# Kernel optimization log

Measured on AMD Instinct MI355X. Metric: run time of the kernel, lower is better.

## Reference

```python
import jax, jax.numpy as jnp
import numpy as np
import math

B, T, C = 2, 2048, 768
N_HEAD, HEAD_DIM = 12, 64
TAU = 1.0
NEG_INF = -1e30  # stand-in for float('-inf') safe under softmax


def setup_inputs() -> dict:
    key = jax.random.key(0)
    k1, k2, k3, k4, k5 = jax.random.split(key, 5)
    hd = N_HEAD * HEAD_DIM
    x = jax.random.normal(k1, (B, T, C), dtype=jnp.float32)
    W_attn = jax.random.normal(k2, (C, 3 * hd), dtype=jnp.float32) * (1.0 / math.sqrt(C))
    b_attn = jnp.zeros((3 * hd,), dtype=jnp.float32)
    W_proj = jax.random.normal(k3, (hd, C), dtype=jnp.float32) * (1.0 / math.sqrt(hd))
    b_proj = jnp.zeros((C,), dtype=jnp.float32)
    return {"x": x, "W_attn": W_attn, "b_attn": b_attn, "W_proj": W_proj, "b_proj": b_proj}


def reference(x, W_attn, b_attn, W_proj, b_proj):
    Bs, Ts, Cs = x.shape
    hd = N_HEAD * HEAD_DIM
    qkv = x @ W_attn + b_attn                                  # [B,T,3*H*hd]
    q, k, v = jnp.split(qkv, 3, axis=2)
    q = q.reshape(Bs, Ts, N_HEAD, HEAD_DIM).transpose(0, 2, 1, 3)  # [B,H,T,d]
    k = k.reshape(Bs, Ts, N_HEAD, HEAD_DIM).transpose(0, 2, 1, 3)
    v = v.reshape(Bs, Ts, N_HEAD, HEAD_DIM).transpose(0, 2, 1, 3)

    att = jnp.einsum('bhtd,bhsd->bhts', q, k) * (1.0 / math.sqrt(HEAD_DIM))
    causal = jnp.tril(jnp.ones((Ts, Ts), dtype=bool))
    att = jnp.where(causal[None, None], att, NEG_INF)          # [B,H,T,T]

    # selection scores from head 0; relu(-inf) == 0 so masked entries vanish
    S = jax.nn.relu(att[:, 0])                                  # [B,T,T]
    # protect_bos_token: zero column 0
    S = S * (jnp.arange(Ts) > 0).astype(S.dtype)[None, None, :]
    # prevent_from_masking_myself: zero diagonal
    S = S * (1.0 - jnp.eye(Ts, dtype=S.dtype))[None]
    # roll rows down by 1 with zero row at the top
    S_shifted = jnp.concatenate([jnp.zeros_like(S[:, :1]), S[:, :-1]], axis=1)
    FF = jnp.cumsum(S_shifted, axis=1)[:, None]                 # [B,1,T,T]
    FF_sum = jnp.clip(FF, 0.0, TAU).sum(axis=-1)                # [B,1,T]
    positions = jnp.arange(Ts, dtype=jnp.float32).reshape(1, 1, Ts, 1)
    M = positions - FF_sum / TAU                                # broadcast -> [1,B,T,T]

    att = jax.nn.softmax(att - FF, axis=-1)
    y = jnp.einsum('bhts,bhsd->bhtd', att, v)
    y = y.transpose(0, 2, 1, 3).reshape(Bs, Ts, hd)
    y = y @ W_proj + b_proj
    return y, M
```

## Files before the change

kernel.cpp:

```cpp
#include <hip/hip_runtime.h>
#include <cstddef>

#define TB   2
#define TT   2048
#define TC   768
#define NHD  12
#define HDD  64
#define QKVN 2304
#define BTM  4096

#define FF_OFF   9437184ull
#define GSUM_OFF 17825792ull
#define FSUM_OFF 17891328ull
#define YATT_OFF 17895424ull
#define YSZ      3145728

typedef __attribute__((ext_vector_type(8))) short bf16x8;
typedef __attribute__((ext_vector_type(4))) float f32x4;

__device__ inline unsigned short f2bf(float f) {
    unsigned u = __float_as_uint(f);
    return (unsigned short)((u + 0x7fffu + ((u >> 16) & 1u)) >> 16);
}

__global__ __launch_bounds__(256) void castbf(
    const float* __restrict__ in, unsigned short* __restrict__ out, int n8)
{
    int idx = blockIdx.x * 256 + threadIdx.x;
    if (idx >= n8) return;
    const float4* p = (const float4*)(in + (size_t)idx * 8);
    float4 a = p[0], b = p[1];
    union { unsigned short us[8]; uint4 u4; } r;
    r.us[0] = f2bf(a.x); r.us[1] = f2bf(a.y); r.us[2] = f2bf(a.z); r.us[3] = f2bf(a.w);
    r.us[4] = f2bf(b.x); r.us[5] = f2bf(b.y); r.us[6] = f2bf(b.z); r.us[7] = f2bf(b.w);
    *(uint4*)(out + (size_t)idx * 8) = r.u4;
}

__global__ __launch_bounds__(256) void tcast(
    const float* __restrict__ W, unsigned short* __restrict__ Wt, int K, int N)
{
    __shared__ unsigned short T[64][80];
    const int tid = threadIdx.x;
    const int k0 = blockIdx.x * 64, n0 = blockIdx.y * 64;
#pragma unroll
    for (int u = 0; u < 4; ++u) {
        int f = u * 256 + tid;
        int kr = f >> 4, nc = (f & 15) * 4;
        float4 v = *(const float4*)(W + (size_t)(k0 + kr) * N + n0 + nc);
        T[nc + 0][kr] = f2bf(v.x); T[nc + 1][kr] = f2bf(v.y);
        T[nc + 2][kr] = f2bf(v.z); T[nc + 3][kr] = f2bf(v.w);
    }
    __syncthreads();
#pragma unroll
    for (int u = 0; u < 2; ++u) {
        int f = u * 256 + tid;
        int nr = f >> 3, kc = (f & 7) * 8;
        *(uint4*)(Wt + (size_t)(n0 + nr) * K + k0 + kc) = *(uint4*)&T[nr][kc];
    }
}

__global__ __launch_bounds__(256) void gemm_bf16(
    const unsigned short* __restrict__ A, const unsigned short* __restrict__ Bt,
    const float* __restrict__ bias, float* __restrict__ C,
    int M, int N, int K)
{
    __shared__ unsigned short As[128 * 64];
    __shared__ unsigned short Bs[128 * 64];
    const int tid = threadIdx.x;
    const int w = tid >> 6, lane = tid & 63;
    const int row0 = blockIdx.y * 128, col0 = blockIdx.x * 128;
    const int moff = (w >> 1) * 64, noff = (w & 1) * 64;
    const int lm = lane & 15, quad = lane >> 4;

    f32x4 acc[4][4];
#pragma unroll
    for (int i = 0; i < 4; ++i)
#pragma unroll
        for (int j = 0; j < 4; ++j) acc[i][j] = (f32x4){0.f, 0.f, 0.f, 0.f};

    for (int k0 = 0; k0 < K; k0 += 64) {
        __syncthreads();
#pragma unroll
        for (int u = 0; u < 4; ++u) {
            int unit = u * 256 + tid;
            int r = unit >> 3, kq = unit & 7;
            int kqs = kq ^ (r & 7);
            bf16x8 va = *(const bf16x8*)(A + (size_t)(row0 + r) * K + k0 + kq * 8);
            *(bf16x8*)&As[r * 64 + kqs * 8] = va;
            bf16x8 vb = *(const bf16x8*)(Bt + (size_t)(col0 + r) * K + k0 + kq * 8);
            *(bf16x8*)&Bs[r * 64 + kqs * 8] = vb;
        }
        __syncthreads();
#pragma unroll
        for (int kh = 0; kh < 2; ++kh) {
            const int kqb = kh * 4 + quad;
            bf16x8 af[4], bfr[4];
#pragma unroll
            for (int i = 0; i < 4; ++i) {
                int mr = moff + i * 16 + lm;
                af[i] = *(const bf16x8*)&As[mr * 64 + (kqb ^ (mr & 7)) * 8];
                int nr = noff + i * 16 + lm;
                bfr[i] = *(const bf16x8*)&Bs[nr * 64 + (kqb ^ (nr & 7)) * 8];
            }
#pragma unroll
            for (int i = 0; i < 4; ++i)
#pragma unroll
                for (int j = 0; j < 4; ++j)
                    acc[i][j] = __builtin_amdgcn_mfma_f32_16x16x32_bf16(
                        af[i], bfr[j], acc[i][j], 0, 0, 0);
        }
    }

#pragma unroll
    for (int j = 0; j < 4; ++j) {
        int n = col0 + noff + j * 16 + lm;
        float bv = bias[n];
#pragma unroll
        for (int i = 0; i < 4; ++i) {
            int mbase = row0 + moff + i * 16 + quad * 4;
#pragma unroll
            for (int r = 0; r < 4; ++r)
                C[(size_t)(mbase + r) * N + n] = acc[i][j][r] + bv;
        }
    }
}

__global__ __launch_bounds__(256) void s_head0_kernel(
    const float* __restrict__ qkv, float* __restrict__ S)
{
    const int tid = threadIdx.x;
    const int tx = tid & 15, ty = tid >> 4;
    const int s0 = blockIdx.x * 64, t0 = blockIdx.y * 64, b = blockIdx.z;

    if (s0 > t0 + 63) {
        float4 z = make_float4(0.f, 0.f, 0.f, 0.f);
#pragma unroll
        for (int i = 0; i < 4; ++i) {
            int t = t0 + ty * 4 + i;
            *(float4*)(S + ((size_t)b * TT + t) * TT + s0 + tx * 4) = z;
        }
        return;
    }

    __shared__ __align__(16) float As[16][68];
    __shared__ __align__(16) float Bs[16][68];
    float acc[4][4];
#pragma unroll
    for (int i = 0; i < 4; ++i)
#pragma unroll
        for (int j = 0; j < 4; ++j) acc[i][j] = 0.f;

    for (int k0 = 0; k0 < 64; k0 += 16) {
        int r = tid >> 2, c = (tid & 3) * 4;
        float4 av = *(const float4*)(qkv + ((size_t)b * TT + t0 + r) * QKVN + k0 + c);
        As[c + 0][r] = av.x; As[c + 1][r] = av.y;
        As[c + 2][r] = av.z; As[c + 3][r] = av.w;
        float4 bv = *(const float4*)(qkv + ((size_t)b * TT + s0 + r) * QKVN + 768 + k0 + c);
        Bs[c + 0][r] = bv.x; Bs[c + 1][r] = bv.y;
        Bs[c + 2][r] = bv.z; Bs[c + 3][r] = bv.w;
        __syncthreads();
#pragma unroll
        for (int kk = 0; kk < 16; ++kk) {
            float4 a4 = *(const float4*)&As[kk][ty * 4];
            float4 b4 = *(const float4*)&Bs[kk][tx * 4];
            float a[4] = {a4.x, a4.y, a4.z, a4.w};
            float bb[4] = {b4.x, b4.y, b4.z, b4.w};
#pragma unroll
            for (int i = 0; i < 4; ++i)
#pragma unroll
                for (int j = 0; j < 4; ++j)
                    acc[i][j] = fmaf(a[i], bb[j], acc[i][j]);
        }
        __syncthreads();
    }

#pragma unroll
    for (int i = 0; i < 4; ++i) {
        int t = t0 + ty * 4 + i;
        int sb = s0 + tx * 4;
        float4 o;
        o.x = (sb + 0 > 0 && sb + 0 < t) ? fmaxf(acc[i][0] * 0.125f, 0.f) : 0.f;
        o.y = (sb + 1 > 0 && sb + 1 < t) ? fmaxf(acc[i][1] * 0.125f, 0.f) : 0.f;
        o.z = (sb + 2 > 0 && sb + 2 < t) ? fmaxf(acc[i][2] * 0.125f, 0.f) : 0.f;
        o.w = (sb + 3 > 0 && sb + 3 < t) ? fmaxf(acc[i][3] * 0.125f, 0.f) : 0.f;
        *(float4*)(S + ((size_t)b * TT + t) * TT + sb) = o;
    }
}

__global__ void scan_pass1(const float* __restrict__ S, float* __restrict__ gsum)
{
    int s = blockIdx.x * 256 + threadIdx.x;
    int g = blockIdx.y, b = blockIdx.z;
    const float* base = S + ((size_t)b * TT + g * 128) * TT + s;
    float acc = 0.f;
#pragma unroll 4
    for (int r = 0; r < 128; ++r) acc += base[(size_t)r * TT];
    gsum[((size_t)b * 16 + g) * TT + s] = acc;
}

__global__ void scan_pass2(float* __restrict__ gsum)
{
    int idx = blockIdx.x * 256 + threadIdx.x;
    int b = idx >> 11, s = idx & 2047;
    float acc = 0.f;
#pragma unroll
    for (int g = 0; g < 16; ++g) {
        size_t a = ((size_t)b * 16 + g) * TT + s;
        float v = gsum[a];
        gsum[a] = acc;
        acc += v;
    }
}

__global__ void scan_pass3(float* __restrict__ S, const float* __restrict__ gsum)
{
    int s = blockIdx.x * 256 + threadIdx.x;
    int g = blockIdx.y, b = blockIdx.z;
    float acc = gsum[((size_t)b * 16 + g) * TT + s];
    float* base = S + ((size_t)b * TT + g * 128) * TT + s;
#pragma unroll 4
    for (int r = 0; r < 128; ++r) {
        float v = base[(size_t)r * TT];
        base[(size_t)r * TT] = acc;
        acc += v;
    }
}

__global__ void ffsum_kernel(const float* __restrict__ FF, float* __restrict__ FS)
{
    int row = blockIdx.x;
    int tid = threadIdx.x;
    const float* p = FF + (size_t)row * TT;
    float acc = 0.f;
#pragma unroll
    for (int s = tid; s < TT; s += 256) {
        float v = p[s];
        acc += fminf(fmaxf(v, 0.f), 1.f);
    }
#pragma unroll
    for (int off = 32; off > 0; off >>= 1) acc += __shfl_down(acc, off, 64);
    __shared__ float red[4];
    if ((tid & 63) == 0) red[tid >> 6] = acc;
    __syncthreads();
    if (tid == 0) FS[row] = (red[0] + red[1]) + (red[2] + red[3]);
}

__global__ void mout_kernel(const float* __restrict__ FS, float* __restrict__ Mo)
{
    size_t idx = (size_t)blockIdx.x * 256 + threadIdx.x;
    int j = (int)(idx & 2047);
    int i = (int)((idx >> 11) & 2047);
    int b = (int)(idx >> 22);
    Mo[idx] = (float)i - FS[b * TT + j];
}

__global__ __launch_bounds__(256) void attn_kernel(
    const float* __restrict__ qkv, const float* __restrict__ FF,
    unsigned short* __restrict__ Yb)
{
    const int sblk = blockIdx.x;
    const int hi = sblk >> 5;
    const int tt = (sblk ^ hi) & 31;
    const int h = hi % NHD;
    const int b = hi / NHD;

    const int tid = threadIdx.x;
    const int w = tid >> 6, lane = tid & 63;
    const int lm = lane & 15, quad = lane >> 4;
    const int t0 = tt * 64;

    __shared__ unsigned short Ks[64 * 64];
    __shared__ unsigned short Vt[64 * 64];
    __shared__ unsigned short Ps[64 * 64];

    const int tq = t0 + w * 16 + lm;
    bf16x8 qf[2];
#pragma unroll
    for (int kh = 0; kh < 2; ++kh) {
        const float* qp = qkv + ((size_t)(b * TT) + tq) * QKVN + h * 64 + kh * 32 + quad * 8;
        float4 a = *(const float4*)qp;
        float4 c = *(const float4*)(qp + 4);
        union { unsigned short us[8]; bf16x8 v; } u;
        u.us[0] = f2bf(a.x); u.us[1] = f2bf(a.y); u.us[2] = f2bf(a.z); u.us[3] = f2bf(a.w);
        u.us[4] = f2bf(c.x); u.us[5] = f2bf(c.y); u.us[6] = f2bf(c.z); u.us[7] = f2bf(c.w);
        qf[kh] = u.v;
    }

    f32x4 accO[4];
#pragma unroll
    for (int j = 0; j < 4; ++j) accO[j] = (f32x4){0.f, 0.f, 0.f, 0.f};
    float m_c = -3.0e38f, l_c = 0.f;

#pragma unroll 1
    for (int it = 0; it <= tt; ++it) {
        const int s0 = it * 64;
        __syncthreads();

#pragma unroll
        for (int u = 0; u < 2; ++u) {
            int unit = u * 256 + tid;
            int r = unit >> 3, kq = unit & 7;
            const float* kp = qkv + ((size_t)(b * TT) + s0 + r) * QKVN + 768 + h * 64 + kq * 8;
            float4 a = *(const float4*)kp;
            float4 c = *(const float4*)(kp + 4);
            union { unsigned short us[8]; bf16x8 v; } uu;
            uu.us[0] = f2bf(a.x); uu.us[1] = f2bf(a.y); uu.us[2] = f2bf(a.z); uu.us[3] = f2bf(a.w);
            uu.us[4] = f2bf(c.x); uu.us[5] = f2bf(c.y); uu.us[6] = f2bf(c.z); uu.us[7] = f2bf(c.w);
            *(bf16x8*)&Ks[r * 64 + (kq ^ (r & 7)) * 8] = uu.v;
        }
        {
            int s = lane;
            const float* vp = qkv + ((size_t)(b * TT) + s0 + s) * QKVN + 1536 + h * 64 + w * 16;
            float4 v0 = *(const float4*)(vp + 0);
            float4 v1 = *(const float4*)(vp + 4);
            float4 v2 = *(const float4*)(vp + 8);
            float4 v3 = *(const float4*)(vp + 12);
            float vv[16] = {v0.x, v0.y, v0.z, v0.w, v1.x, v1.y, v1.z, v1.w,
                            v2.x, v2.y, v2.z, v2.w, v3.x, v3.y, v3.z, v3.w};
            const int sg = s >> 3, sl = s & 7;
#pragma unroll
            for (int dd = 0; dd < 16; ++dd) {
                int d = w * 16 + dd;
                Vt[d * 64 + (sg ^ (d & 7)) * 8 + sl] = f2bf(vv[dd]);
            }
        }
        __syncthreads();

        f32x4 accS[4];
#pragma unroll
        for (int mi = 0; mi < 4; ++mi) accS[mi] = (f32x4){0.f, 0.f, 0.f, 0.f};
#pragma unroll
        for (int kh = 0; kh < 2; ++kh)
#pragma unroll
            for (int mi = 0; mi < 4; ++mi) {
                int sr = mi * 16 + lm;
                bf16x8 kf = *(const bf16x8*)&Ks[sr * 64 + ((kh * 4 + quad) ^ (sr & 7)) * 8];
                accS[mi] = __builtin_amdgcn_mfma_f32_16x16x32_bf16(kf, qf[kh], accS[mi], 0, 0, 0);
            }

        float sc[4][4];
        float rm = -3.0e38f;
        const float* ffrow = FF + ((size_t)(b * TT) + tq) * TT + s0;
#pragma unroll
        for (int mi = 0; mi < 4; ++mi) {
            float4 f4 = *(const float4*)(ffrow + mi * 16 + quad * 4);
            float fa[4] = {f4.x, f4.y, f4.z, f4.w};
#pragma unroll
            for (int r = 0; r < 4; ++r) {
                float v = accS[mi][r] * 0.125f - fa[r];
                if (it == tt && s0 + mi * 16 + quad * 4 + r > tq) v = -3.0e38f;
                sc[mi][r] = v;
                rm = fmaxf(rm, v);
            }
        }
        rm = fmaxf(rm, __shfl_xor(rm, 16, 64));
        rm = fmaxf(rm, __shfl_xor(rm, 32, 64));
        float mnew = fmaxf(m_c, rm);
        float alpha = __expf(m_c - mnew);
        m_c = mnew;
        float rs = 0.f;
#pragma unroll
        for (int mi = 0; mi < 4; ++mi)
#pragma unroll
            for (int r = 0; r < 4; ++r) {
                float p = __expf(sc[mi][r] - mnew);
                sc[mi][r] = p;
                rs += p;
            }
        rs += __shfl_xor(rs, 16, 64);
        rs += __shfl_xor(rs, 32, 64);
        l_c = l_c * alpha + rs;

        float a_r[4];
#pragma unroll
        for (int r = 0; r < 4; ++r) a_r[r] = __shfl(alpha, quad * 4 + r, 64);
#pragma unroll
        for (int nj = 0; nj < 4; ++nj)
#pragma unroll
            for (int r = 0; r < 4; ++r) accO[nj][r] *= a_r[r];

        const int qrow = w * 16 + lm;
#pragma unroll
        for (int mi = 0; mi < 4; ++mi)
#pragma unroll
            for (int r = 0; r < 4; ++r) {
                int sr = mi * 16 + quad * 4 + r;
                Ps[qrow * 64 + ((sr >> 3) ^ (qrow & 7)) * 8 + (sr & 7)] = f2bf(sc[mi][r]);
            }

        bf16x8 pf[2];
#pragma unroll
        for (int kh = 0; kh < 2; ++kh)
            pf[kh] = *(const bf16x8*)&Ps[qrow * 64 + ((kh * 4 + quad) ^ (qrow & 7)) * 8];
#pragma unroll
        for (int kh = 0; kh < 2; ++kh)
#pragma unroll
            for (int nj = 0; nj < 4; ++nj) {
                int dr = nj * 16 + lm;
                bf16x8 vf = *(const bf16x8*)&Vt[dr * 64 + ((kh * 4 + quad) ^ (dr & 7)) * 8];
                accO[nj] = __builtin_amdgcn_mfma_f32_16x16x32_bf16(pf[kh], vf, accO[nj], 0, 0, 0);
            }
    }

    float l_r[4];
#pragma unroll
    for (int r = 0; r < 4; ++r) l_r[r] = __shfl(l_c, quad * 4 + r, 64);
#pragma unroll
    for (int nj = 0; nj < 4; ++nj)
#pragma unroll
        for (int r = 0; r < 4; ++r) {
            int trow = t0 + w * 16 + quad * 4 + r;
            Yb[((size_t)(b * TT) + trow) * TC + h * 64 + nj * 16 + lm] =
                f2bf(accO[nj][r] / l_r[r]);
        }
}

extern "C" void kernel_launch(void* const* d_in, const int* in_sizes, int n_in,
                              void* d_out, int out_size, void* d_ws, size_t ws_size,
                              hipStream_t stream)
{
    const float* x      = (const float*)d_in[0];
    const float* W_attn = (const float*)d_in[1];
    const float* b_attn = (const float*)d_in[2];
    const float* W_proj = (const float*)d_in[3];
    const float* b_proj = (const float*)d_in[4];
    float* out = (float*)d_out;
    float* ws  = (float*)d_ws;

    float* qkv  = ws;
    float* FFb  = ws + FF_OFF;
    float* gsum = ws + GSUM_OFF;
    float* fsum = ws + FSUM_OFF;

    unsigned short* xb  = (unsigned short*)(ws + FF_OFF);
    unsigned short* WtA = xb + (size_t)BTM * TC;
    unsigned short* WtP = (unsigned short*)(ws + FF_OFF);
    unsigned short* ytb = (unsigned short*)(ws + YATT_OFF);

    castbf<<<dim3(1536), dim3(256), 0, stream>>>(x, xb, BTM * TC / 8);
    tcast<<<dim3(TC / 64, QKVN / 64), dim3(256), 0, stream>>>(W_attn, WtA, TC, QKVN);

    gemm_bf16<<<dim3(QKVN / 128, BTM / 128), dim3(256), 0, stream>>>(
        xb, WtA, b_attn, qkv, BTM, QKVN, TC);

    s_head0_kernel<<<dim3(TT / 64, TT / 64, TB), dim3(256), 0, stream>>>(qkv, FFb);

    scan_pass1<<<dim3(TT / 256, 16, TB), dim3(256), 0, stream>>>(FFb, gsum);
    scan_pass2<<<dim3(TB * TT / 256), dim3(256), 0, stream>>>(gsum);
    scan_pass3<<<dim3(TT / 256, 16, TB), dim3(256), 0, stream>>>(FFb, gsum);

    ffsum_kernel<<<dim3(TB * TT), dim3(256), 0, stream>>>(FFb, fsum);

    attn_kernel<<<dim3(TT / 64 * NHD * TB), dim3(256), 0, stream>>>(qkv, FFb, ytb);

    tcast<<<dim3(TC / 64, TC / 64), dim3(256), 0, stream>>>(W_proj, WtP, TC, TC);

    gemm_bf16<<<dim3(TC / 128, BTM / 128), dim3(256), 0, stream>>>(
        ytb, WtP, b_proj, out, BTM, TC, TC);

    mout_kernel<<<dim3((unsigned)((size_t)TB * TT * TT / 256)), dim3(256), 0, stream>>>(
        fsum, out + YSZ);
}
```

Baseline: 299.6 us.

## Fuse scan partial sums and clip-sum into S and scan kernels, widen attention tiles

The head-0 score kernel now uses bf16 MFMA and emits per-64-row column partial sums, which removes the separate scan_pass1 read of the full S matrix. The clip-and-sum row reduction is folded into scan_pass3 through wave shuffles and atomics, so the ffsum kernel and its extra pass over FF are gone. The attention kernel processes 128 query rows per block with two sub-tiles per wave, halving K/V staging per query and scheduling the heaviest blocks first. Risks are lower precision in S (bf16 instead of fp32 FMA), heavy atomic traffic on fsum, and fewer attention blocks (384) for occupancy.

```diff
diff --git a/kernel.cpp b/kernel.cpp
--- a/kernel.cpp
+++ b/kernel.cpp
@@ -10,9 +10,9 @@
 #define BTM  4096
 
 #define FF_OFF   9437184ull
-#define GSUM_OFF 17825792ull
-#define FSUM_OFF 17891328ull
-#define YATT_OFF 17895424ull
+#define YTB_OFF  17825792ull
+#define GSUM_OFF 19398656ull
+#define FSUM_OFF 19529728ull
 #define YSZ      3145728
 
 typedef __attribute__((ext_vector_type(8))) short bf16x8;
@@ -126,123 +126,124 @@
 }
 
 __global__ __launch_bounds__(256) void s_head0_kernel(
-    const float* __restrict__ qkv, float* __restrict__ S)
-{
+    const float* __restrict__ qkv, float* __restrict__ S, float* __restrict__ gsum)
+{
+    const int s0 = blockIdx.x * 64, t0 = blockIdx.y * 64, b = blockIdx.z;
     const int tid = threadIdx.x;
-    const int tx = tid & 15, ty = tid >> 4;
-    const int s0 = blockIdx.x * 64, t0 = blockIdx.y * 64, b = blockIdx.z;
-
-    if (s0 > t0 + 63) {
+    const int w = tid >> 6, lane = tid & 63;
+    const int lm = lane & 15, quad = lane >> 4;
+
+    if (s0 > t0) {
         float4 z = make_float4(0.f, 0.f, 0.f, 0.f);
 #pragma unroll
         for (int i = 0; i < 4; ++i) {
-            int t = t0 + ty * 4 + i;
-            *(float4*)(S + ((size_t)b * TT + t) * TT + s0 + tx * 4) = z;
-        }
+            int f = i * 256 + tid;
+            int r = f >> 4, c = (f & 15) * 4;
+            *(float4*)(S + ((size_t)b * TT + t0 + r) * TT + s0 + c) = z;
+        }
+        if (tid < 64) gsum[((size_t)b * 32 + blockIdx.y) * TT + s0 + tid] = 0.f;
         return;
     }
 
-    __shared__ __align__(16) float As[16][68];
-    __shared__ __align__(16) float Bs[16][68];
-    float acc[4][4];
-#pragma unroll
-    for (int i = 0; i < 4; ++i)
-#pragma unroll
-        for (int j = 0; j < 4; ++j) acc[i][j] = 0.f;
-
-    for (int k0 = 0; k0 < 64; k0 += 16) {
-        int r = tid >> 2, c = (tid & 3) * 4;
-        float4 av = *(const float4*)(qkv + ((size_t)b * TT + t0 + r) * QKVN + k0 + c);
-        As[c + 0][r] = av.x; As[c + 1][r] = av.y;
-        As[c + 2][r] = av.z; As[c + 3][r] = av.w;
-        float4 bv = *(const float4*)(qkv + ((size_t)b * TT + s0 + r) * QKVN + 768 + k0 + c);
-        Bs[c + 0][r] = bv.x; Bs[c + 1][r] = bv.y;
-        Bs[c + 2][r] = bv.z; Bs[c + 3][r] = bv.w;
-        __syncthreads();
-#pragma unroll
-        for (int kk = 0; kk < 16; ++kk) {
-            float4 a4 = *(const float4*)&As[kk][ty * 4];
-            float4 b4 = *(const float4*)&Bs[kk][tx * 4];
-            float a[4] = {a4.x, a4.y, a4.z, a4.w};
-            float bb[4] = {b4.x, b4.y, b4.z, b4.w};
-#pragma unroll
-            for (int i = 0; i < 4; ++i)
-#pragma unroll
-                for (int j = 0; j < 4; ++j)
-                    acc[i][j] = fmaf(a[i], bb[j], acc[i][j]);
-        }
-        __syncthreads();
-    }
-
-#pragma unroll
-    for (int i = 0; i < 4; ++i) {
-        int t = t0 + ty * 4 + i;
-        int sb = s0 + tx * 4;
-        float4 o;
-        o.x = (sb + 0 > 0 && sb + 0 < t) ? fmaxf(acc[i][0] * 0.125f, 0.f) : 0.f;
-        o.y = (sb + 1 > 0 && sb + 1 < t) ? fmaxf(acc[i][1] * 0.125f, 0.f) : 0.f;
-        o.z = (sb + 2 > 0 && sb + 2 < t) ? fmaxf(acc[i][2] * 0.125f, 0.f) : 0.f;
-        o.w = (sb + 3 > 0 && sb + 3 < t) ? fmaxf(acc[i][3] * 0.125f, 0.f) : 0.f;
-        *(float4*)(S + ((size_t)b * TT + t) * TT + sb) = o;
-    }
-}
-
-__global__ void scan_pass1(const float* __restrict__ S, float* __restrict__ gsum)
-{
-    int s = blockIdx.x * 256 + threadIdx.x;
-    int g = blockIdx.y, b = blockIdx.z;
-    const float* base = S + ((size_t)b * TT + g * 128) * TT + s;
-    float acc = 0.f;
-#pragma unroll 4
-    for (int r = 0; r < 128; ++r) acc += base[(size_t)r * TT];
-    gsum[((size_t)b * 16 + g) * TT + s] = acc;
-}
-
-__global__ void scan_pass2(float* __restrict__ gsum)
+    __shared__ unsigned short Ks[64 * 64];
+    __shared__ float colpart[4][64];
+
+#pragma unroll
+    for (int u = 0; u < 2; ++u) {
+        int unit = u * 256 + tid;
+        int r = unit >> 3, kq = unit & 7;
+        const float* kp = qkv + ((size_t)(b * TT) + s0 + r) * QKVN + 768 + kq * 8;
+        float4 a = *(const float4*)kp;
+        float4 c = *(const float4*)(kp + 4);
+        union { unsigned short us[8]; bf16x8 v; } uu;
+        uu.us[0] = f2bf(a.x); uu.us[1] = f2bf(a.y); uu.us[2] = f2bf(a.z); uu.us[3] = f2bf(a.w);
+        uu.us[4] = f2bf(c.x); uu.us[5] = f2bf(c.y); uu.us[6] = f2bf(c.z); uu.us[7] = f2bf(c.w);
+        *(bf16x8*)&Ks[r * 64 + (kq ^ (r & 7)) * 8] = uu.v;
+    }
+    bf16x8 af[2];
+#pragma unroll
+    for (int kh = 0; kh < 2; ++kh) {
+        const float* qp = qkv + ((size_t)(b * TT) + t0 + w * 16 + lm) * QKVN + kh * 32 + quad * 8;
+        float4 a = *(const float4*)qp;
+        float4 c = *(const float4*)(qp + 4);
+        union { unsigned short us[8]; bf16x8 v; } uu;
+        uu.us[0] = f2bf(a.x); uu.us[1] = f2bf(a.y); uu.us[2] = f2bf(a.z); uu.us[3] = f2bf(a.w);
+        uu.us[4] = f2bf(c.x); uu.us[5] = f2bf(c.y); uu.us[6] = f2bf(c.z); uu.us[7] = f2bf(c.w);
+        af[kh] = uu.v;
+    }
+    __syncthreads();
+
+    f32x4 acc[4];
+#pragma unroll
+    for (int nj = 0; nj < 4; ++nj) acc[nj] = (f32x4){0.f, 0.f, 0.f, 0.f};
+#pragma unroll
+    for (int kh = 0; kh < 2; ++kh)
+#pragma unroll
+        for (int nj = 0; nj < 4; ++nj) {
+            int sr = nj * 16 + lm;
+            bf16x8 kb = *(const bf16x8*)&Ks[sr * 64 + ((kh * 4 + quad) ^ (sr & 7)) * 8];
+            acc[nj] = __builtin_amdgcn_mfma_f32_16x16x32_bf16(af[kh], kb, acc[nj], 0, 0, 0);
+        }
+
+#pragma unroll
+    for (int nj = 0; nj < 4; ++nj) {
+        int s = s0 + nj * 16 + lm;
+        float cs = 0.f;
+#pragma unroll
+        for (int r = 0; r < 4; ++r) {
+            int t = t0 + w * 16 + quad * 4 + r;
+            float v = (s > 0 && s < t) ? fmaxf(acc[nj][r] * 0.125f, 0.f) : 0.f;
+            S[((size_t)b * TT + t) * TT + s] = v;
+            cs += v;
+        }
+        cs += __shfl_xor(cs, 16, 64);
+        cs += __shfl_xor(cs, 32, 64);
+        if (quad == 0) colpart[w][nj * 16 + lm] = cs;
+    }
+    __syncthreads();
+    if (tid < 64) {
+        float g = colpart[0][tid] + colpart[1][tid] + colpart[2][tid] + colpart[3][tid];
+        gsum[((size_t)b * 32 + blockIdx.y) * TT + s0 + tid] = g;
+    }
+}
+
+__global__ void scan_pass2(float* __restrict__ gsum, float* __restrict__ fsum)
 {
     int idx = blockIdx.x * 256 + threadIdx.x;
     int b = idx >> 11, s = idx & 2047;
+    fsum[idx] = 0.f;
     float acc = 0.f;
 #pragma unroll
-    for (int g = 0; g < 16; ++g) {
-        size_t a = ((size_t)b * 16 + g) * TT + s;
+    for (int g = 0; g < 32; ++g) {
+        size_t a = ((size_t)b * 32 + g) * TT + s;
         float v = gsum[a];
         gsum[a] = acc;
         acc += v;
     }
 }
 
-__global__ void scan_pass3(float* __restrict__ S, const float* __restrict__ gsum)
+__global__ void scan_pass3(float* __restrict__ S, const float* __restrict__ gsum,
+                           float* __restrict__ fsum)
 {
     int s = blockIdx.x * 256 + threadIdx.x;
     int g = blockIdx.y, b = blockIdx.z;
-    float acc = gsum[((size_t)b * 16 + g) * TT + s];
-    float* base = S + ((size_t)b * TT + g * 128) * TT + s;
-#pragma unroll 4
-    for (int r = 0; r < 128; ++r) {
+    int lane = threadIdx.x & 63;
+    float acc = gsum[((size_t)b * 32 + g) * TT + s];
+    float* base = S + ((size_t)b * TT + g * 64) * TT + s;
+#pragma unroll 2
+    for (int r = 0; r < 64; ++r) {
         float v = base[(size_t)r * TT];
         base[(size_t)r * TT] = acc;
+        float c = fminf(fmaxf(acc, 0.f), 1.f);
+        c += __shfl_xor(c, 1, 64);
+        c += __shfl_xor(c, 2, 64);
+        c += __shfl_xor(c, 4, 64);
+        c += __shfl_xor(c, 8, 64);
+        c += __shfl_xor(c, 16, 64);
+        c += __shfl_xor(c, 32, 64);
+        if (lane == 0) atomicAdd(&fsum[(size_t)b * TT + g * 64 + r], c);
         acc += v;
     }
-}
-
-__global__ void ffsum_kernel(const float* __restrict__ FF, float* __restrict__ FS)
-{
-    int row = blockIdx.x;
-    int tid = threadIdx.x;
-    const float* p = FF + (size_t)row * TT;
-    float acc = 0.f;
-#pragma unroll
-    for (int s = tid; s < TT; s += 256) {
-        float v = p[s];
-        acc += fminf(fmaxf(v, 0.f), 1.f);
-    }
-#pragma unroll
-    for (int off = 32; off > 0; off >>= 1) acc += __shfl_down(acc, off, 64);
-    __shared__ float red[4];
-    if ((tid & 63) == 0) red[tid >> 6] = acc;
-    __syncthreads();
-    if (tid == 0) FS[row] = (red[0] + red[1]) + (red[2] + red[3]);
 }
 
 __global__ void mout_kernel(const float* __restrict__ FS, float* __restrict__ Mo)
@@ -258,41 +259,47 @@
     const float* __restrict__ qkv, const float* __restrict__ FF,
     unsigned short* __restrict__ Yb)
 {
-    const int sblk = blockIdx.x;
-    const int hi = sblk >> 5;
-    const int tt = (sblk ^ hi) & 31;
-    const int h = hi % NHD;
-    const int b = hi / NHD;
+    const int x = blockIdx.x;
+    const int qb = 15 - x / 24;
+    const int bh = x % 24;
+    const int h = bh % NHD, b = bh / NHD;
+    const int t0 = qb * 128;
 
     const int tid = threadIdx.x;
     const int w = tid >> 6, lane = tid & 63;
     const int lm = lane & 15, quad = lane >> 4;
-    const int t0 = tt * 64;
 
     __shared__ unsigned short Ks[64 * 64];
     __shared__ unsigned short Vt[64 * 64];
-    __shared__ unsigned short Ps[64 * 64];
-
-    const int tq = t0 + w * 16 + lm;
-    bf16x8 qf[2];
-#pragma unroll
-    for (int kh = 0; kh < 2; ++kh) {
-        const float* qp = qkv + ((size_t)(b * TT) + tq) * QKVN + h * 64 + kh * 32 + quad * 8;
-        float4 a = *(const float4*)qp;
-        float4 c = *(const float4*)(qp + 4);
-        union { unsigned short us[8]; bf16x8 v; } u;
-        u.us[0] = f2bf(a.x); u.us[1] = f2bf(a.y); u.us[2] = f2bf(a.z); u.us[3] = f2bf(a.w);
-        u.us[4] = f2bf(c.x); u.us[5] = f2bf(c.y); u.us[6] = f2bf(c.z); u.us[7] = f2bf(c.w);
-        qf[kh] = u.v;
-    }
-
-    f32x4 accO[4];
-#pragma unroll
-    for (int j = 0; j < 4; ++j) accO[j] = (f32x4){0.f, 0.f, 0.f, 0.f};
-    float m_c = -3.0e38f, l_c = 0.f;
-
+    __shared__ unsigned short Ps[128 * 64];
+
+    bf16x8 qf[2][2];
+    int tq[2];
+#pragma unroll
+    for (int qs = 0; qs < 2; ++qs) {
+        tq[qs] = t0 + w * 32 + qs * 16 + lm;
+#pragma unroll
+        for (int kh = 0; kh < 2; ++kh) {
+            const float* qp = qkv + ((size_t)(b * TT) + tq[qs]) * QKVN + h * 64 + kh * 32 + quad * 8;
+            float4 a = *(const float4*)qp;
+            float4 c = *(const float4*)(qp + 4);
+            union { unsigned short us[8]; bf16x8 v; } u;
+            u.us[0] = f2bf(a.x); u.us[1] = f2bf(a.y); u.us[2] = f2bf(a.z); u.us[3] = f2bf(a.w);
+            u.us[4] = f2bf(c.x); u.us[5] = f2bf(c.y); u.us[6] = f2bf(c.z); u.us[7] = f2bf(c.w);
+            qf[qs][kh] = u.v;
+        }
+    }
+
+    f32x4 accO[2][4];
+#pragma unroll
+    for (int m = 0; m < 2; ++m)
+#pragma unroll
+        for (int j = 0; j < 4; ++j) accO[m][j] = (f32x4){0.f, 0.f, 0.f, 0.f};
+    float m_c[2] = {-3.0e38f, -3.0e38f}, l_c[2] = {0.f, 0.f};
+
+    const int ntile = qb * 2 + 2;
 #pragma unroll 1
-    for (int it = 0; it <= tt; ++it) {
+    for (int it = 0; it < ntile; ++it) {
         const int s0 = it * 64;
         __syncthreads();
 
@@ -326,93 +333,110 @@
         }
         __syncthreads();
 
-        f32x4 accS[4];
-#pragma unroll
-        for (int mi = 0; mi < 4; ++mi) accS[mi] = (f32x4){0.f, 0.f, 0.f, 0.f};
-#pragma unroll
-        for (int kh = 0; kh < 2; ++kh)
+        float alpha[2];
+#pragma unroll
+        for (int qs = 0; qs < 2; ++qs) {
+            f32x4 accS[4];
+#pragma unroll
+            for (int mi = 0; mi < 4; ++mi) accS[mi] = (f32x4){0.f, 0.f, 0.f, 0.f};
+#pragma unroll
+            for (int kh = 0; kh < 2; ++kh)
+#pragma unroll
+                for (int mi = 0; mi < 4; ++mi) {
+                    int sr = mi * 16 + lm;
+                    bf16x8 kf = *(const bf16x8*)&Ks[sr * 64 + ((kh * 4 + quad) ^ (sr & 7)) * 8];
+                    accS[mi] = __builtin_amdgcn_mfma_f32_16x16x32_bf16(kf, qf[qs][kh], accS[mi], 0, 0, 0);
+                }
+
+            float sc[4][4];
+            float rm = -3.0e38f;
+            const float* ffrow = FF + ((size_t)(b * TT) + tq[qs]) * TT + s0;
+            const bool diag = (it >= qb * 2);
 #pragma unroll
             for (int mi = 0; mi < 4; ++mi) {
-                int sr = mi * 16 + lm;
-                bf16x8 kf = *(const bf16x8*)&Ks[sr * 64 + ((kh * 4 + quad) ^ (sr & 7)) * 8];
-                accS[mi] = __builtin_amdgcn_mfma_f32_16x16x32_bf16(kf, qf[kh], accS[mi], 0, 0, 0);
-            }
-
-        float sc[4][4];
-        float rm = -3.0e38f;
-        const float* ffrow = FF + ((size_t)(b * TT) + tq) * TT + s0;
-#pragma unroll
-        for (int mi = 0; mi < 4; ++mi) {
-            float4 f4 = *(const float4*)(ffrow + mi * 16 + quad * 4);
-            float fa[4] = {f4.x, f4.y, f4.z, f4.w};
-#pragma unroll
-            for (int r = 0; r < 4; ++r) {
-                float v = accS[mi][r] * 0.125f - fa[r];
-                if (it == tt && s0 + mi * 16 + quad * 4 + r > tq) v = -3.0e38f;
-                sc[mi][r] = v;
-                rm = fmaxf(rm, v);
-            }
-        }
-        rm = fmaxf(rm, __shfl_xor(rm, 16, 64));
-        rm = fmaxf(rm, __shfl_xor(rm, 32, 64));
-        float mnew = fmaxf(m_c, rm);
-        float alpha = __expf(m_c - mnew);
-        m_c = mnew;
-        float rs = 0.f;
-#pragma unroll
-        for (int mi = 0; mi < 4; ++mi)
-#pragma unroll
-            for (int r = 0; r < 4; ++r) {
-                float p = __expf(sc[mi][r] - mnew);
-                sc[mi][r] = p;
-                rs += p;
-            }
-        rs += __shfl_xor(rs, 16, 64);
-        rs += __shfl_xor(rs, 32, 64);
-        l_c = l_c * alpha + rs;
-
-        float a_r[4];
-#pragma unroll
-        for (int r = 0; r < 4; ++r) a_r[r] = __shfl(alpha, quad * 4 + r, 64);
-#pragma unroll
-        for (int nj = 0; nj < 4; ++nj)
-#pragma unroll
-            for (int r = 0; r < 4; ++r) accO[nj][r] *= a_r[r];
-
-        const int qrow = w * 16 + lm;
-#pragma unroll
-        for (int mi = 0; mi < 4; ++mi)
-#pragma unroll
-            for (int r = 0; r < 4; ++r) {
-                int sr = mi * 16 + quad * 4 + r;
-                Ps[qrow * 64 + ((sr >> 3) ^ (qrow & 7)) * 8 + (sr & 7)] = f2bf(sc[mi][r]);
-            }
-
-        bf16x8 pf[2];
-#pragma unroll
-        for (int kh = 0; kh < 2; ++kh)
-            pf[kh] = *(const bf16x8*)&Ps[qrow * 64 + ((kh * 4 + quad) ^ (qrow & 7)) * 8];
+                float4 f4 = *(const float4*)(ffrow + mi * 16 + quad * 4);
+                float fa[4] = {f4.x, f4.y, f4.z, f4.w};
+#pragma unroll
+                for (int r = 0; r < 4; ++r) {
+                    float v = accS[mi][r] * 0.125f - fa[r];
+                    if (diag && s0 + mi * 16 + quad * 4 + r > tq[qs]) v = -3.0e38f;
+                    sc[mi][r] = v;
+                    rm = fmaxf(rm, v);
+                }
+            }
+            rm = fmaxf(rm, __shfl_xor(rm, 16, 64));
+            rm = fmaxf(rm, __shfl_xor(rm, 32, 64));
+            float mnew = fmaxf(m_c[qs], rm);
+            alpha[qs] = __expf(m_c[qs] - mnew);
+            m_c[qs] = mnew;
+            float rs = 0.f;
+#pragma unroll
+            for (int mi = 0; mi < 4; ++mi)
+#pragma unroll
+                for (int r = 0; r < 4; ++r) {
+                    float p = __expf(sc[mi][r] - mnew);
+                    sc[mi][r] = p;
+                    rs += p;
+                }
+            rs += __shfl_xor(rs, 16, 64);
+            rs += __shfl_xor(rs, 32, 64);
+            l_c[qs] = l_c[qs] * alpha[qs] + rs;
+
+            const int qrow = w * 32 + qs * 16 + lm;
+#pragma unroll
+            for (int mi = 0; mi < 4; ++mi)
+#pragma unroll
+                for (int r = 0; r < 4; ++r) {
+                    int sr = mi * 16 + quad * 4 + r;
+                    Ps[qrow * 64 + ((sr >> 3) ^ (qrow & 7)) * 8 + (sr & 7)] = f2bf(sc[mi][r]);
+                }
+        }
+
+#pragma unroll
+        for (int m = 0; m < 2; ++m) {
+            float a_r[4];
+#pragma unroll
+            for (int r = 0; r < 4; ++r) a_r[r] = __shfl(alpha[m], quad * 4 + r, 64);
+#pragma unroll
+            for (int nj = 0; nj < 4; ++nj)
+#pragma unroll
+                for (int r = 0; r < 4; ++r) accO[m][nj][r] *= a_r[r];
+        }
+
+        bf16x8 pf[2][2];
+#pragma unroll
+        for (int m = 0; m < 2; ++m)
+#pragma unroll
+            for (int kh = 0; kh < 2; ++kh) {
+                int qrow = w * 32 + m * 16 + lm;
+                pf[m][kh] = *(const bf16x8*)&Ps[qrow * 64 + ((kh * 4 + quad) ^ (qrow & 7)) * 8];
+            }
 #pragma unroll
         for (int kh = 0; kh < 2; ++kh)
 #pragma unroll
             for (int nj = 0; nj < 4; ++nj) {
                 int dr = nj * 16 + lm;
                 bf16x8 vf = *(const bf16x8*)&Vt[dr * 64 + ((kh * 4 + quad) ^ (dr & 7)) * 8];
-                accO[nj] = __builtin_amdgcn_mfma_f32_16x16x32_bf16(pf[kh], vf, accO[nj], 0, 0, 0);
-            }
-    }
-
-    float l_r[4];
-#pragma unroll
-    for (int r = 0; r < 4; ++r) l_r[r] = __shfl(l_c, quad * 4 + r, 64);
-#pragma unroll
-    for (int nj = 0; nj < 4; ++nj)
-#pragma unroll
-        for (int r = 0; r < 4; ++r) {
-            int trow = t0 + w * 16 + quad * 4 + r;
-            Yb[((size_t)(b * TT) + trow) * TC + h * 64 + nj * 16 + lm] =
-                f2bf(accO[nj][r] / l_r[r]);
-        }
+#pragma unroll
+                for (int m = 0; m < 2; ++m)
+                    accO[m][nj] = __builtin_amdgcn_mfma_f32_16x16x32_bf16(pf[m][kh], vf, accO[m][nj], 0, 0, 0);
+            }
+    }
+
+#pragma unroll
+    for (int m = 0; m < 2; ++m) {
+        float l_r[4];
+#pragma unroll
+        for (int r = 0; r < 4; ++r) l_r[r] = __shfl(l_c[m], quad * 4 + r, 64);
+#pragma unroll
+        for (int nj = 0; nj < 4; ++nj)
+#pragma unroll
+            for (int r = 0; r < 4; ++r) {
+                int trow = t0 + w * 32 + m * 16 + quad * 4 + r;
+                Yb[((size_t)(b * TT) + trow) * TC + h * 64 + nj * 16 + lm] =
+                    f2bf(accO[m][nj][r] / l_r[r]);
+            }
+    }
 }
 
 extern "C" void kernel_launch(void* const* d_in, const int* in_sizes, int n_in,
@@ -435,7 +459,7 @@
     unsigned short* xb  = (unsigned short*)(ws + FF_OFF);
     unsigned short* WtA = xb + (size_t)BTM * TC;
     unsigned short* WtP = (unsigned short*)(ws + FF_OFF);
-    unsigned short* ytb = (unsigned short*)(ws + YATT_OFF);
+    unsigned short* ytb = (unsigned short*)(ws + YTB_OFF);
 
     castbf<<<dim3(1536), dim3(256), 0, stream>>>(x, xb, BTM * TC / 8);
     tcast<<<dim3(TC / 64, QKVN / 64), dim3(256), 0, stream>>>(W_attn, WtA, TC, QKVN);
@@ -443,15 +467,12 @@
     gemm_bf16<<<dim3(QKVN / 128, BTM / 128), dim3(256), 0, stream>>>(
         xb, WtA, b_attn, qkv, BTM, QKVN, TC);
 
-    s_head0_kernel<<<dim3(TT / 64, TT / 64, TB), dim3(256), 0, stream>>>(qkv, FFb);
-
-    scan_pass1<<<dim3(TT / 256, 16, TB), dim3(256), 0, stream>>>(FFb, gsum);
-    scan_pass2<<<dim3(TB * TT / 256), dim3(256), 0, stream>>>(gsum);
-    scan_pass3<<<dim3(TT / 256, 16, TB), dim3(256), 0, stream>>>(FFb, gsum);
-
-    ffsum_kernel<<<dim3(TB * TT), dim3(256), 0, stream>>>(FFb, fsum);
-
-    attn_kernel<<<dim3(TT / 64 * NHD * TB), dim3(256), 0, stream>>>(qkv, FFb, ytb);
+    s_head0_kernel<<<dim3(TT / 64, TT / 64, TB), dim3(256), 0, stream>>>(qkv, FFb, gsum);
+
+    scan_pass2<<<dim3(TB * TT / 256), dim3(256), 0, stream>>>(gsum, fsum);
+    scan_pass3<<<dim3(TT / 256, 32, TB), dim3(256), 0, stream>>>(FFb, gsum, fsum);
+
+    attn_kernel<<<dim3(16 * NHD * TB), dim3(256), 0, stream>>>(qkv, FFb, ytb);
 
     tcast<<<dim3(TC / 64, TC / 64), dim3(256), 0, stream>>>(W_proj, WtP, TC, TC);
 
```

Measured after the change: 309.1 us. 3.2% more time.

## Store QKV as bf16, use MFMA for head-0 scores, fuse scan pass1

Applied to the files above, without the earlier changes.

The QKV GEMM now writes bf16 output directly, so attention and the selection-score kernels load bf16 without per-element conversion and QKV traffic is halved. The head-0 score kernel is rewritten to use bf16 MFMA instead of scalar FP32 FMAs, and it emits per-64-row column partial sums, which removes the separate scan_pass1 read over the full S matrix. The scan now uses 32 groups of 64 rows. The trade-off is that head-0 scores are computed from bf16-rounded q/k, which affects the precision of FF and M.

```diff
diff --git a/kernel.cpp b/kernel.cpp
--- a/kernel.cpp
+++ b/kernel.cpp
@@ -10,9 +10,9 @@
 #define BTM  4096
 
 #define FF_OFF   9437184ull
-#define GSUM_OFF 17825792ull
-#define FSUM_OFF 17891328ull
-#define YATT_OFF 17895424ull
+#define YTB_OFF  17825792ull
+#define GSUM_OFF 19398656ull
+#define FSUM_OFF 19529728ull
 #define YSZ      3145728
 
 typedef __attribute__((ext_vector_type(8))) short bf16x8;
@@ -59,10 +59,11 @@
     }
 }
 
+template <bool BF16OUT>
 __global__ __launch_bounds__(256) void gemm_bf16(
     const unsigned short* __restrict__ A, const unsigned short* __restrict__ Bt,
     const float* __restrict__ bias, float* __restrict__ C,
-    int M, int N, int K)
+    unsigned short* __restrict__ Cb, int M, int N, int K)
 {
     __shared__ unsigned short As[128 * 64];
     __shared__ unsigned short Bs[128 * 64];
@@ -119,83 +120,86 @@
         for (int i = 0; i < 4; ++i) {
             int mbase = row0 + moff + i * 16 + quad * 4;
 #pragma unroll
-            for (int r = 0; r < 4; ++r)
-                C[(size_t)(mbase + r) * N + n] = acc[i][j][r] + bv;
+            for (int r = 0; r < 4; ++r) {
+                float v = acc[i][j][r] + bv;
+                if (BF16OUT)
+                    Cb[(size_t)(mbase + r) * N + n] = f2bf(v);
+                else
+                    C[(size_t)(mbase + r) * N + n] = v;
+            }
         }
     }
 }
 
 __global__ __launch_bounds__(256) void s_head0_kernel(
-    const float* __restrict__ qkv, float* __restrict__ S)
-{
+    const unsigned short* __restrict__ qkvb, float* __restrict__ S,
+    float* __restrict__ gsum)
+{
+    const int s0 = blockIdx.x * 64, t0 = blockIdx.y * 64, b = blockIdx.z;
     const int tid = threadIdx.x;
-    const int tx = tid & 15, ty = tid >> 4;
-    const int s0 = blockIdx.x * 64, t0 = blockIdx.y * 64, b = blockIdx.z;
-
-    if (s0 > t0 + 63) {
+    const int w = tid >> 6, lane = tid & 63;
+    const int lm = lane & 15, quad = lane >> 4;
+
+    if (s0 > t0) {
         float4 z = make_float4(0.f, 0.f, 0.f, 0.f);
 #pragma unroll
         for (int i = 0; i < 4; ++i) {
-            int t = t0 + ty * 4 + i;
-            *(float4*)(S + ((size_t)b * TT + t) * TT + s0 + tx * 4) = z;
-        }
+            int f = i * 256 + tid;
+            int r = f >> 4, c = (f & 15) * 4;
+            *(float4*)(S + ((size_t)b * TT + t0 + r) * TT + s0 + c) = z;
+        }
+        if (tid < 64) gsum[((size_t)b * 32 + blockIdx.y) * TT + s0 + tid] = 0.f;
         return;
     }
 
-    __shared__ __align__(16) float As[16][68];
-    __shared__ __align__(16) float Bs[16][68];
-    float acc[4][4];
-#pragma unroll
-    for (int i = 0; i < 4; ++i)
-#pragma unroll
-        for (int j = 0; j < 4; ++j) acc[i][j] = 0.f;
-
-    for (int k0 = 0; k0 < 64; k0 += 16) {
-        int r = tid >> 2, c = (tid & 3) * 4;
-        float4 av = *(const float4*)(qkv + ((size_t)b * TT + t0 + r) * QKVN + k0 + c);
-        As[c + 0][r] = av.x; As[c + 1][r] = av.y;
-        As[c + 2][r] = av.z; As[c + 3][r] = av.w;
-        float4 bv = *(const float4*)(qkv + ((size_t)b * TT + s0 + r) * QKVN + 768 + k0 + c);
-        Bs[c + 0][r] = bv.x; Bs[c + 1][r] = bv.y;
-        Bs[c + 2][r] = bv.z; Bs[c + 3][r] = bv.w;
-        __syncthreads();
-#pragma unroll
-        for (int kk = 0; kk < 16; ++kk) {
-            float4 a4 = *(const float4*)&As[kk][ty * 4];
-            float4 b4 = *(const float4*)&Bs[kk][tx * 4];
-            float a[4] = {a4.x, a4.y, a4.z, a4.w};
-            float bb[4] = {b4.x, b4.y, b4.z, b4.w};
-#pragma unroll
-            for (int i = 0; i < 4; ++i)
-#pragma unroll
-                for (int j = 0; j < 4; ++j)
-                    acc[i][j] = fmaf(a[i], bb[j], acc[i][j]);
-        }
-        __syncthreads();
-    }
-
-#pragma unroll
-    for (int i = 0; i < 4; ++i) {
-        int t = t0 + ty * 4 + i;
-        int sb = s0 + tx * 4;
-        float4 o;
-        o.x = (sb + 0 > 0 && sb + 0 < t) ? fmaxf(acc[i][0] * 0.125f, 0.f) : 0.f;
-        o.y = (sb + 1 > 0 && sb + 1 < t) ? fmaxf(acc[i][1] * 0.125f, 0.f) : 0.f;
-        o.z = (sb + 2 > 0 && sb + 2 < t) ? fmaxf(acc[i][2] * 0.125f, 0.f) : 0.f;
-        o.w = (sb + 3 > 0 && sb + 3 < t) ? fmaxf(acc[i][3] * 0.125f, 0.f) : 0.f;
-        *(float4*)(S + ((size_t)b * TT + t) * TT + sb) = o;
-    }
-}
-
-__global__ void scan_pass1(const float* __restrict__ S, float* __restrict__ gsum)
-{
-    int s = blockIdx.x * 256 + threadIdx.x;
-    int g = blockIdx.y, b = blockIdx.z;
-    const float* base = S + ((size_t)b * TT + g * 128) * TT + s;
-    float acc = 0.f;
-#pragma unroll 4
-    for (int r = 0; r < 128; ++r) acc += base[(size_t)r * TT];
-    gsum[((size_t)b * 16 + g) * TT + s] = acc;
+    __shared__ unsigned short Ks[64 * 64];
+    __shared__ float colpart[4][64];
+
+#pragma unroll
+    for (int u = 0; u < 2; ++u) {
+        int unit = u * 256 + tid;
+        int r = unit >> 3, kq = unit & 7;
+        bf16x8 kv = *(const bf16x8*)(qkvb + ((size_t)(b * TT) + s0 + r) * QKVN + 768 + kq * 8);
+        *(bf16x8*)&Ks[r * 64 + (kq ^ (r & 7)) * 8] = kv;
+    }
+    bf16x8 af[2];
+#pragma unroll
+    for (int kh = 0; kh < 2; ++kh)
+        af[kh] = *(const bf16x8*)(qkvb + ((size_t)(b * TT) + t0 + w * 16 + lm) * QKVN + kh * 32 + quad * 8);
+    __syncthreads();
+
+    f32x4 acc[4];
+#pragma unroll
+    for (int nj = 0; nj < 4; ++nj) acc[nj] = (f32x4){0.f, 0.f, 0.f, 0.f};
+#pragma unroll
+    for (int kh = 0; kh < 2; ++kh)
+#pragma unroll
+        for (int nj = 0; nj < 4; ++nj) {
+            int sr = nj * 16 + lm;
+            bf16x8 kb = *(const bf16x8*)&Ks[sr * 64 + ((kh * 4 + quad) ^ (sr & 7)) * 8];
+            acc[nj] = __builtin_amdgcn_mfma_f32_16x16x32_bf16(af[kh], kb, acc[nj], 0, 0, 0);
+        }
+
+#pragma unroll
+    for (int nj = 0; nj < 4; ++nj) {
+        int s = s0 + nj * 16 + lm;
+        float cs = 0.f;
+#pragma unroll
+        for (int r = 0; r < 4; ++r) {
+            int t = t0 + w * 16 + quad * 4 + r;
+            float v = (s > 0 && s < t) ? fmaxf(acc[nj][r] * 0.125f, 0.f) : 0.f;
+            S[((size_t)b * TT + t) * TT + s] = v;
+            cs += v;
+        }
+        cs += __shfl_xor(cs, 16, 64);
+        cs += __shfl_xor(cs, 32, 64);
+        if (quad == 0) colpart[w][nj * 16 + lm] = cs;
+    }
+    __syncthreads();
+    if (tid < 64) {
+        float g = colpart[0][tid] + colpart[1][tid] + colpart[2][tid] + colpart[3][tid];
+        gsum[((size_t)b * 32 + blockIdx.y) * TT + s0 + tid] = g;
+    }
 }
 
 __global__ void scan_pass2(float* __restrict__ gsum)
@@ -204,8 +208,8 @@
     int b = idx >> 11, s = idx & 2047;
     float acc = 0.f;
 #pragma unroll
-    for (int g = 0; g < 16; ++g) {
-        size_t a = ((size_t)b * 16 + g) * TT + s;
+    for (int g = 0; g < 32; ++g) {
+        size_t a = ((size_t)b * 32 + g) * TT + s;
         float v = gsum[a];
         gsum[a] = acc;
         acc += v;
@@ -216,10 +220,10 @@
 {
     int s = blockIdx.x * 256 + threadIdx.x;
     int g = blockIdx.y, b = blockIdx.z;
-    float acc = gsum[((size_t)b * 16 + g) * TT + s];
-    float* base = S + ((size_t)b * TT + g * 128) * TT + s;
+    float acc = gsum[((size_t)b * 32 + g) * TT + s];
+    float* base = S + ((size_t)b * TT + g * 64) * TT + s;
 #pragma unroll 4
-    for (int r = 0; r < 128; ++r) {
+    for (int r = 0; r < 64; ++r) {
         float v = base[(size_t)r * TT];
         base[(size_t)r * TT] = acc;
         acc += v;
@@ -255,7 +259,7 @@
 }
 
 __global__ __launch_bounds__(256) void attn_kernel(
-    const float* __restrict__ qkv, const float* __restrict__ FF,
+    const unsigned short* __restrict__ qkvb, const float* __restrict__ FF,
     unsigned short* __restrict__ Yb)
 {
     const int sblk = blockIdx.x;
@@ -276,15 +280,8 @@
     const int tq = t0 + w * 16 + lm;
     bf16x8 qf[2];
 #pragma unroll
-    for (int kh = 0; kh < 2; ++kh) {
-        const float* qp = qkv + ((size_t)(b * TT) + tq) * QKVN + h * 64 + kh * 32 + quad * 8;
-        float4 a = *(const float4*)qp;
-        float4 c = *(const float4*)(qp + 4);
-        union { unsigned short us[8]; bf16x8 v; } u;
-        u.us[0] = f2bf(a.x); u.us[1] = f2bf(a.y); u.us[2] = f2bf(a.z); u.us[3] = f2bf(a.w);
-        u.us[4] = f2bf(c.x); u.us[5] = f2bf(c.y); u.us[6] = f2bf(c.z); u.us[7] = f2bf(c.w);
-        qf[kh] = u.v;
-    }
+    for (int kh = 0; kh < 2; ++kh)
+        qf[kh] = *(const bf16x8*)(qkvb + ((size_t)(b * TT) + tq) * QKVN + h * 64 + kh * 32 + quad * 8);
 
     f32x4 accO[4];
 #pragma unroll
@@ -300,28 +297,25 @@
         for (int u = 0; u < 2; ++u) {
             int unit = u * 256 + tid;
             int r = unit >> 3, kq = unit & 7;
-            const float* kp = qkv + ((size_t)(b * TT) + s0 + r) * QKVN + 768 + h * 64 + kq * 8;
-            float4 a = *(const float4*)kp;
-            float4 c = *(const float4*)(kp + 4);
-            union { unsigned short us[8]; bf16x8 v; } uu;
-            uu.us[0] = f2bf(a.x); uu.us[1] = f2bf(a.y); uu.us[2] = f2bf(a.z); uu.us[3] = f2bf(a.w);
-            uu.us[4] = f2bf(c.x); uu.us[5] = f2bf(c.y); uu.us[6] = f2bf(c.z); uu.us[7] = f2bf(c.w);
-            *(bf16x8*)&Ks[r * 64 + (kq ^ (r & 7)) * 8] = uu.v;
+            bf16x8 kv = *(const bf16x8*)(qkvb + ((size_t)(b * TT) + s0 + r) * QKVN + 768 + h * 64 + kq * 8);
+            *(bf16x8*)&Ks[r * 64 + (kq ^ (r & 7)) * 8] = kv;
         }
         {
             int s = lane;
-            const float* vp = qkv + ((size_t)(b * TT) + s0 + s) * QKVN + 1536 + h * 64 + w * 16;
-            float4 v0 = *(const float4*)(vp + 0);
-            float4 v1 = *(const float4*)(vp + 4);
-            float4 v2 = *(const float4*)(vp + 8);
-            float4 v3 = *(const float4*)(vp + 12);
-            float vv[16] = {v0.x, v0.y, v0.z, v0.w, v1.x, v1.y, v1.z, v1.w,
-                            v2.x, v2.y, v2.z, v2.w, v3.x, v3.y, v3.z, v3.w};
+            const unsigned short* vp = qkvb + ((size_t)(b * TT) + s0 + s) * QKVN + 1536 + h * 64 + w * 16;
+            union { uint4 u4; unsigned short us[8]; } a, c;
+            a.u4 = *(const uint4*)vp;
+            c.u4 = *(const uint4*)(vp + 8);
             const int sg = s >> 3, sl = s & 7;
 #pragma unroll
-            for (int dd = 0; dd < 16; ++dd) {
+            for (int dd = 0; dd < 8; ++dd) {
                 int d = w * 16 + dd;
-                Vt[d * 64 + (sg ^ (d & 7)) * 8 + sl] = f2bf(vv[dd]);
+                Vt[d * 64 + (sg ^ (d & 7)) * 8 + sl] = a.us[dd];
+            }
+#pragma unroll
+            for (int dd = 8; dd < 16; ++dd) {
+                int d = w * 16 + dd;
+                Vt[d * 64 + (sg ^ (d & 7)) * 8 + sl] = c.us[dd - 8];
             }
         }
         __syncthreads();
@@ -427,7 +421,7 @@
     float* out = (float*)d_out;
     float* ws  = (float*)d_ws;
 
-    float* qkv  = ws;
+    unsigned short* qkvb = (unsigned short*)ws;
     float* FFb  = ws + FF_OFF;
     float* gsum = ws + GSUM_OFF;
     float* fsum = ws + FSUM_OFF;
@@ -435,28 +429,27 @@
     unsigned short* xb  = (unsigned short*)(ws + FF_OFF);
     unsigned short* WtA = xb + (size_t)BTM * TC;
     unsigned short* WtP = (unsigned short*)(ws + FF_OFF);
-    unsigned short* ytb = (unsigned short*)(ws + YATT_OFF);
+    unsigned short* ytb = (unsigned short*)(ws + YTB_OFF);
 
     castbf<<<dim3(1536), dim3(256), 0, stream>>>(x, xb, BTM * TC / 8);
     tcast<<<dim3(TC / 64, QKVN / 64), dim3(256), 0, stream>>>(W_attn, WtA, TC, QKVN);
 
-    gemm_bf16<<<dim3(QKVN / 128, BTM / 128), dim3(256), 0, stream>>>(
-        xb, WtA, b_attn, qkv, BTM, QKVN, TC);
-
-    s_head0_kernel<<<dim3(TT / 64, TT / 64, TB), dim3(256), 0, stream>>>(qkv, FFb);
-
-    scan_pass1<<<dim3(TT / 256, 16, TB), dim3(256), 0, stream>>>(FFb, gsum);
+    gemm_bf16<true><<<dim3(QKVN / 128, BTM / 128), dim3(256), 0, stream>>>(
+        xb, WtA, b_attn, nullptr, qkvb, BTM, QKVN, TC);
+
+    s_head0_kernel<<<dim3(TT / 64, TT / 64, TB), dim3(256), 0, stream>>>(qkvb, FFb, gsum);
+
     scan_pass2<<<dim3(TB * TT / 256), dim3(256), 0, stream>>>(gsum);
-    scan_pass3<<<dim3(TT / 256, 16, TB), dim3(256), 0, stream>>>(FFb, gsum);
+    scan_pass3<<<dim3(TT / 256, 32, TB), dim3(256), 0, stream>>>(FFb, gsum);
 
     ffsum_kernel<<<dim3(TB * TT), dim3(256), 0, stream>>>(FFb, fsum);
 
-    attn_kernel<<<dim3(TT / 64 * NHD * TB), dim3(256), 0, stream>>>(qkv, FFb, ytb);
+    attn_kernel<<<dim3(TT / 64 * NHD * TB), dim3(256), 0, stream>>>(qkvb, FFb, ytb);
 
     tcast<<<dim3(TC / 64, TC / 64), dim3(256), 0, stream>>>(W_proj, WtP, TC, TC);
 
-    gemm_bf16<<<dim3(TC / 128, BTM / 128), dim3(256), 0, stream>>>(
-        ytb, WtP, b_proj, out, BTM, TC, TC);
+    gemm_bf16<false><<<dim3(TC / 128, BTM / 128), dim3(256), 0, stream>>>(
+        ytb, WtP, b_proj, out, nullptr, BTM, TC, TC);
 
     mout_kernel<<<dim3((unsigned)((size_t)TB * TT * TT / 256)), dim3(256), 0, stream>>>(
         fsum, out + YSZ);
```

Result: faster. 258.2 us (-13.8%).
